# Optimization experiments

Measured on AMD Instinct MI355X. Metric: run time of the kernel, lower is better.

Reference implementation:

```python
import jax, jax.numpy as jnp
import numpy as np

DIM = 1024
N_HEADS = 16
HEAD_DIM = DIM // N_HEADS
D_FF = 4096
EPS = 1e-6


def setup_inputs() -> dict:
    key = jax.random.key(0)
    ks = jax.random.split(key, 8)
    B, S = 2, 2048
    s = 0.02
    return {
        "x": jax.random.normal(ks[0], (B, S, DIM), dtype=jnp.float32),
        "mask": jnp.ones((B, 1, S, S), dtype=bool),
        "wq": jax.random.normal(ks[1], (DIM, DIM), dtype=jnp.float32) * s,
        "wk": jax.random.normal(ks[2], (DIM, DIM), dtype=jnp.float32) * s,
        "wv": jax.random.normal(ks[3], (DIM, DIM), dtype=jnp.float32) * s,
        "wo": jax.random.normal(ks[4], (DIM, DIM), dtype=jnp.float32) * s,
        "w_up": jax.random.normal(ks[5], (DIM, D_FF), dtype=jnp.float32) * s,
        "b_up": jnp.zeros((D_FF,), dtype=jnp.float32),
        "w_down": jax.random.normal(ks[6], (D_FF, DIM), dtype=jnp.float32) * s,
        "b_down": jnp.zeros((DIM,), dtype=jnp.float32),
        "ln1_a": jnp.ones((DIM,), dtype=jnp.float32),
        "ln1_b": jnp.zeros((DIM,), dtype=jnp.float32),
        "ln2_a": jnp.ones((DIM,), dtype=jnp.float32),
        "ln2_b": jnp.zeros((DIM,), dtype=jnp.float32),
    }


def _layernorm(x, alpha, bias):
    mu = jnp.mean(x, axis=-1, keepdims=True)
    # torch .std() is unbiased (ddof=1); denominator is (std + eps)
    sig = jnp.std(x, axis=-1, keepdims=True, ddof=1)
    return alpha * (x - mu) / (sig + EPS) + bias


def _attention(h, wq, wk, wv, wo):
    B, S, _ = h.shape
    q = (h @ wq).reshape(B, S, N_HEADS, HEAD_DIM).transpose(0, 2, 1, 3)
    k = (h @ wk).reshape(B, S, N_HEADS, HEAD_DIM).transpose(0, 2, 1, 3)
    v = (h @ wv).reshape(B, S, N_HEADS, HEAD_DIM).transpose(0, 2, 1, 3)
    scores = jnp.einsum("bhqd,bhkd->bhqk", q, k) / jnp.sqrt(jnp.float32(HEAD_DIM))
    # NOTE: original's masked_fill result is discarded -> mask is a no-op
    probs = jax.nn.softmax(scores, axis=-1)
    out = jnp.einsum("bhqk,bhkd->bhqd", probs, v)
    out = out.transpose(0, 2, 1, 3).reshape(B, S, DIM)
    return out @ wo


def reference(x, mask, wq, wk, wv, wo, w_up, b_up, w_down, b_down,
              ln1_a, ln1_b, ln2_a, ln2_b):
    h = _layernorm(x, ln1_a, ln1_b)
    x = x + _attention(h, wq, wk, wv, wo)
    h = _layernorm(x, ln2_a, ln2_b)
    ff = (jax.nn.relu(h @ w_up + b_up)) @ w_down + b_down
    return x + ff
```

## Files before the change

### kernel.cpp

```cpp
#include <hip/hip_runtime.h>
#include <hip/hip_bf16.h>

typedef __bf16 bf16_t;
typedef __bf16 bf16x8 __attribute__((ext_vector_type(8)));
typedef __bf16 bf16x4 __attribute__((ext_vector_type(4)));
typedef float  f32x4  __attribute__((ext_vector_type(4)));

#define DIM   1024
#define NHEAD 16
#define HD    64
#define DFF   4096
#define SEQ   2048
#define NTOK  4096

__device__ __forceinline__ void gl_lds16(const bf16_t* g, bf16_t* l) {
  __builtin_amdgcn_global_load_lds(
      (const __attribute__((address_space(1))) void*)g,
      (__attribute__((address_space(3))) void*)l, 16, 0, 0);
}

struct P4 { const float* a; const float* b; const float* c; const float* d; };

__global__ __launch_bounds__(256)
void transpose_cvt4(P4 in, bf16_t* __restrict__ out) {
  __shared__ bf16_t tile[32][33];
  const int z = blockIdx.z;
  const float* src = (z == 0) ? in.a : (z == 1) ? in.b : (z == 2) ? in.c : in.d;
  bf16_t* dst = out + (long)z * DIM * DIM;
  const int bx = blockIdx.x * 32, by = blockIdx.y * 32;
  const int t = threadIdx.x;
  const int r = t >> 3, c4 = (t & 7) * 4;
  f32x4 v = *(const f32x4*)&src[(long)(by + r) * DIM + bx + c4];
  tile[r][c4 + 0] = (bf16_t)v[0]; tile[r][c4 + 1] = (bf16_t)v[1];
  tile[r][c4 + 2] = (bf16_t)v[2]; tile[r][c4 + 3] = (bf16_t)v[3];
  __syncthreads();
  bf16x4 w;
  w[0] = tile[c4 + 0][r]; w[1] = tile[c4 + 1][r];
  w[2] = tile[c4 + 2][r]; w[3] = tile[c4 + 3][r];
  *(bf16x4*)&dst[(long)(bx + r) * DIM + by + c4] = w;
}

__global__ __launch_bounds__(256)
void transpose_cvt(const float* __restrict__ in, bf16_t* __restrict__ out,
                   int M, int N) {
  __shared__ bf16_t tile[32][33];
  const int bx = blockIdx.x * 32, by = blockIdx.y * 32;
  const int t = threadIdx.x;
  const int r = t >> 3, c4 = (t & 7) * 4;
  f32x4 v = *(const f32x4*)&in[(long)(by + r) * N + bx + c4];
  tile[r][c4 + 0] = (bf16_t)v[0]; tile[r][c4 + 1] = (bf16_t)v[1];
  tile[r][c4 + 2] = (bf16_t)v[2]; tile[r][c4 + 3] = (bf16_t)v[3];
  __syncthreads();
  bf16x4 w;
  w[0] = tile[c4 + 0][r]; w[1] = tile[c4 + 1][r];
  w[2] = tile[c4 + 2][r]; w[3] = tile[c4 + 3][r];
  *(bf16x4*)&out[(long)(bx + r) * M + by + c4] = w;
}

__global__ __launch_bounds__(256)
void layernorm_k(const float* __restrict__ x, const float* __restrict__ a,
                 const float* __restrict__ b, bf16_t* __restrict__ out) {
  const int row = blockIdx.x;
  const int t   = threadIdx.x;
  const float* xr = x + (long)row * DIM;
  f32x4 v = *(const f32x4*)&xr[t * 4];
  float s1 = v[0] + v[1] + v[2] + v[3];
  float s2 = v[0]*v[0] + v[1]*v[1] + v[2]*v[2] + v[3]*v[3];
  #pragma unroll
  for (int off = 32; off > 0; off >>= 1) {
    s1 += __shfl_down(s1, off);
    s2 += __shfl_down(s2, off);
  }
  __shared__ float r1[4], r2[4];
  if ((t & 63) == 0) { r1[t >> 6] = s1; r2[t >> 6] = s2; }
  __syncthreads();
  s1 = r1[0] + r1[1] + r1[2] + r1[3];
  s2 = r2[0] + r2[1] + r2[2] + r2[3];
  const float mu = s1 * (1.0f / DIM);
  float var = (s2 - (float)DIM * mu * mu) * (1.0f / (DIM - 1));
  var = fmaxf(var, 0.0f);
  const float inv = 1.0f / (sqrtf(var) + 1e-6f);
  f32x4 av = *(const f32x4*)&a[t * 4];
  f32x4 bv = *(const f32x4*)&b[t * 4];
  bf16x4 o;
  o[0] = (bf16_t)(av[0] * (v[0] - mu) * inv + bv[0]);
  o[1] = (bf16_t)(av[1] * (v[1] - mu) * inv + bv[1]);
  o[2] = (bf16_t)(av[2] * (v[2] - mu) * inv + bv[2]);
  o[3] = (bf16_t)(av[3] * (v[3] - mu) * inv + bv[3]);
  *(bf16x4*)&out[(long)row * DIM + t * 4] = o;
}

enum { EPI_QKV = 1, EPI_RES = 2, EPI_BIAS_RELU = 3, EPI_BIAS_RES = 4 };

#define BM 128
#define BK 32

template <int EPI, int TBN>
__global__ __launch_bounds__(256)
void gemm_bt(const bf16_t* __restrict__ A, int lda,
             const bf16_t* __restrict__ BT, int ldb,
             bf16_t* __restrict__ Cb, float* __restrict__ Cf,
             bf16_t* __restrict__ Cb2,
             const float* __restrict__ res,
             const float* __restrict__ bias,
             int M, int N, int K) {
  __shared__ bf16_t sA[2][BM][BK];
  __shared__ bf16_t sB[2][TBN][BK];
  const int tid  = threadIdx.x;
  const int m0   = blockIdx.y * BM;
  const int n0   = blockIdx.x * TBN;
  const int lane = tid & 63, wave = tid >> 6;
  constexpr int MI = (TBN == 128) ? 4 : 2;
  const int wm = (TBN == 128) ? (wave >> 1) * 64 : wave * 32;
  const int wn = (TBN == 128) ? (wave & 1) * 64 : 0;
  const int fm = lane & 15, fq = lane >> 4;

  const int lr = lane >> 2, lc = (lane & 3) * 8;
  const bf16_t* gA0 = &A[(long)(m0 + wave * 32 + lr) * lda + lc];
  const bf16_t* gA1 = gA0 + 16 * (long)lda;
  const int brow = (TBN == 128) ? wave * 32 : wave * 16;
  const bf16_t* gB0 = &BT[(long)(n0 + brow + lr) * ldb + lc];
  const bf16_t* gB1 = gB0 + 16 * (long)ldb;

  f32x4 acc[MI][4] = {};

  gl_lds16(gA0, &sA[0][wave * 32][0]);
  gl_lds16(gA1, &sA[0][wave * 32 + 16][0]);
  gl_lds16(gB0, &sB[0][brow][0]);
  if (TBN == 128) gl_lds16(gB1, &sB[0][wave * 32 + 16][0]);
  gA0 += BK; gA1 += BK; gB0 += BK; gB1 += BK;

  int p = 0;
  for (int k0 = 0; k0 < K; k0 += BK, p ^= 1) {
    __syncthreads();
    if (k0 + BK < K) {
      gl_lds16(gA0, &sA[p ^ 1][wave * 32][0]);
      gl_lds16(gA1, &sA[p ^ 1][wave * 32 + 16][0]);
      gl_lds16(gB0, &sB[p ^ 1][brow][0]);
      if (TBN == 128) gl_lds16(gB1, &sB[p ^ 1][wave * 32 + 16][0]);
      gA0 += BK; gA1 += BK; gB0 += BK; gB1 += BK;
    }
    bf16x8 af[MI], bfr[4];
    #pragma unroll
    for (int i = 0; i < MI; i++) af[i]  = *(const bf16x8*)&sA[p][wm + i * 16 + fm][fq * 8];
    #pragma unroll
    for (int j = 0; j < 4; j++)  bfr[j] = *(const bf16x8*)&sB[p][wn + j * 16 + fm][fq * 8];
    #pragma unroll
    for (int i = 0; i < MI; i++)
      #pragma unroll
      for (int j = 0; j < 4; j++)
        acc[i][j] = __builtin_amdgcn_mfma_f32_16x16x32_bf16(af[i], bfr[j], acc[i][j], 0, 0, 0);
  }

  #pragma unroll
  for (int i = 0; i < MI; i++) {
    #pragma unroll
    for (int j = 0; j < 4; j++) {
      const int mb = m0 + wm + i * 16 + fq * 4;
      const int n  = n0 + wn + j * 16 + fm;
      #pragma unroll
      for (int r = 0; r < 4; r++) {
        const int m = mb + r;
        float vv = acc[i][j][r];
        if constexpr (EPI == EPI_QKV) {
          const int mat = n >> 10, h_ = (n >> 6) & 15, d_ = n & 63;
          const int b_ = m >> 11, s_ = m & 2047;
          if (mat == 2) {
            Cb2[((long)(b_ * NHEAD + h_) * HD + d_) * SEQ + s_] = (bf16_t)vv;
          } else {
            Cb[(long)mat * (32L * SEQ * HD) + (((long)(b_ * NHEAD + h_)) * SEQ + s_) * HD + d_] = (bf16_t)vv;
          }
        } else if constexpr (EPI == EPI_RES) {
          Cf[(long)m * N + n] = vv + res[(long)m * N + n];
        } else if constexpr (EPI == EPI_BIAS_RELU) {
          Cb[(long)m * N + n] = (bf16_t)fmaxf(vv + bias[n], 0.0f);
        } else {
          Cf[(long)m * N + n] = vv + bias[n] + res[(long)m * N + n];
        }
      }
    }
  }
}

#define KVT 128

__global__ __launch_bounds__(256)
void flash_attn(const bf16_t* __restrict__ q, const bf16_t* __restrict__ k,
                const bf16_t* __restrict__ vt, bf16_t* __restrict__ attn) {
  __shared__ bf16_t sK[16 * 64 * 8];
  __shared__ bf16_t sV[16 * 64 * 8];

  const int tid  = threadIdx.x;
  const int qb   = blockIdx.x & 15, bh = blockIdx.x >> 4;
  const int b    = bh >> 4, h = bh & 15;
  const int lane = tid & 63, wave = tid >> 6;
  const int fm   = lane & 15, fq = lane >> 4;
  const int qw0  = qb * 128 + wave * 32;

  const bf16_t* qh  = q  + (long)bh * SEQ * HD;
  const bf16_t* kh  = k  + (long)bh * SEQ * HD;
  const bf16_t* vth = vt + (long)bh * HD * SEQ;

  bf16x8 bQ[2][2];
  #pragma unroll
  for (int qt = 0; qt < 2; qt++)
    #pragma unroll
    for (int kk = 0; kk < 2; kk++) {
      bf16x8 v = *(const bf16x8*)&qh[(long)(qw0 + qt * 16 + fm) * HD + kk * 32 + fq * 8];
      #pragma unroll
      for (int e = 0; e < 8; e++) v[e] = (bf16_t)((float)v[e] * 0.125f);
      bQ[qt][kk] = v;
    }

  float la = 0.f, lb = 0.f;
  f32x4 oA[4] = {}, oB[4] = {};

  for (int kv0 = 0; kv0 < SEQ; kv0 += KVT) {
    __syncthreads();
    #pragma unroll
    for (int p = 0; p < 4; p++) {
      const int id = tid + p * 256;
      {
        const int rho = id >> 3, c0 = (id & 7) * 8;
        const int u = rho >> 5, w = rho & 31;
        const int h2 = (w >> 2) & 1;
        const int fmw = ((w >> 3) << 2) | (w & 3);
        const int kk = (id >> 2) & 1, fq3 = id & 3;
        bf16x8 g = *(const bf16x8*)&kh[(long)(kv0 + rho) * HD + c0];
        *(bf16x8*)&sK[(((u * 2 + h2) * 2 + kk) * 64 + fq3 * 16 + fmw) * 8] = g;
      }
      {
        const int d = id >> 4, c0 = (id & 15) * 8;
        const int u = c0 >> 5, fq3 = (c0 >> 3) & 3;
        const int jd = d >> 4, fmw = d & 15;
        bf16x8 g = *(const bf16x8*)&vth[(long)d * SEQ + kv0 + c0];
        *(bf16x8*)&sV[((u * 4 + jd) * 64 + fq3 * 16 + fmw) * 8] = g;
      }
    }
    __syncthreads();

    #pragma unroll
    for (int u = 0; u < 4; u++) {
      f32x4 stA[2], stB[2];
      #pragma unroll
      for (int h2 = 0; h2 < 2; h2++) {
        bf16x8 aK0 = *(const bf16x8*)&sK[(((u * 2 + h2) * 2 + 0) * 64 + lane) * 8];
        bf16x8 aK1 = *(const bf16x8*)&sK[(((u * 2 + h2) * 2 + 1) * 64 + lane) * 8];
        f32x4 z0 = {};
        z0 = __builtin_amdgcn_mfma_f32_16x16x32_bf16(aK0, bQ[0][0], z0, 0, 0, 0);
        stA[h2] = __builtin_amdgcn_mfma_f32_16x16x32_bf16(aK1, bQ[0][1], z0, 0, 0, 0);
        f32x4 z1 = {};
        z1 = __builtin_amdgcn_mfma_f32_16x16x32_bf16(aK0, bQ[1][0], z1, 0, 0, 0);
        stB[h2] = __builtin_amdgcn_mfma_f32_16x16x32_bf16(aK1, bQ[1][1], z1, 0, 0, 0);
      }
      bf16x8 pA, pB;
      #pragma unroll
      for (int h2 = 0; h2 < 2; h2++)
        #pragma unroll
        for (int r = 0; r < 4; r++) {
          const float ea = __expf(stA[h2][r]);
          const float eb = __expf(stB[h2][r]);
          la += ea; lb += eb;
          pA[h2 * 4 + r] = (bf16_t)ea;
          pB[h2 * 4 + r] = (bf16_t)eb;
        }
      #pragma unroll
      for (int jd = 0; jd < 4; jd++) {
        bf16x8 bV = *(const bf16x8*)&sV[((u * 4 + jd) * 64 + lane) * 8];
        oA[jd] = __builtin_amdgcn_mfma_f32_16x16x32_bf16(pA, bV, oA[jd], 0, 0, 0);
        oB[jd] = __builtin_amdgcn_mfma_f32_16x16x32_bf16(pB, bV, oB[jd], 0, 0, 0);
      }
    }
  }

  la += __shfl_xor(la, 16); la += __shfl_xor(la, 32);
  lb += __shfl_xor(lb, 16); lb += __shfl_xor(lb, 32);
  float invA[4], invB[4];
  #pragma unroll
  for (int r = 0; r < 4; r++) {
    const int src = (fq * 4 + r) * 4;
    invA[r] = 1.0f / __int_as_float(__builtin_amdgcn_ds_bpermute(src, __float_as_int(la)));
    invB[r] = 1.0f / __int_as_float(__builtin_amdgcn_ds_bpermute(src, __float_as_int(lb)));
  }

  #pragma unroll
  for (int r = 0; r < 4; r++) {
    const long rowA = ((long)b * SEQ + qw0 + fq * 4 + r) * DIM + h * HD;
    const long rowB = rowA + 16L * DIM;
    #pragma unroll
    for (int jd = 0; jd < 4; jd++) {
      attn[rowA + jd * 16 + fm] = (bf16_t)(oA[jd][r] * invA[r]);
      attn[rowB + jd * 16 + fm] = (bf16_t)(oB[jd][r] * invB[r]);
    }
  }
}

extern "C" void kernel_launch(void* const* d_in, const int* in_sizes, int n_in,
                              void* d_out, int out_size, void* d_ws, size_t ws_size,
                              hipStream_t stream) {
  (void)in_sizes; (void)n_in; (void)out_size; (void)ws_size;
  const float* x      = (const float*)d_in[0];
  const float* wq     = (const float*)d_in[2];
  const float* wk     = (const float*)d_in[3];
  const float* wv     = (const float*)d_in[4];
  const float* wo     = (const float*)d_in[5];
  const float* w_up   = (const float*)d_in[6];
  const float* b_up   = (const float*)d_in[7];
  const float* w_down = (const float*)d_in[8];
  const float* b_down = (const float*)d_in[9];
  const float* ln1a   = (const float*)d_in[10];
  const float* ln1b   = (const float*)d_in[11];
  const float* ln2a   = (const float*)d_in[12];
  const float* ln2b   = (const float*)d_in[13];

  char* ws = (char*)d_ws;
  const size_t MB = 1ull << 20;
  bf16_t* wqkvT  = (bf16_t*)(ws);
  bf16_t* woT    = (bf16_t*)(ws + 6 * MB);
  bf16_t* h      = (bf16_t*)(ws + 8 * MB);
  bf16_t* attn   = (bf16_t*)(ws + 8 * MB);
  bf16_t* qkv    = (bf16_t*)(ws + 16 * MB);
  bf16_t* qd     = (bf16_t*)(ws + 16 * MB);
  bf16_t* kd     = (bf16_t*)(ws + 24 * MB);
  bf16_t* vtd    = (bf16_t*)(ws + 32 * MB);
  float*  x1     = (float*)(ws + 40 * MB);
  bf16_t* h2     = (bf16_t*)(ws + 0 * MB);
  bf16_t* wupT   = (bf16_t*)(ws + 56 * MB);
  bf16_t* wdownT = (bf16_t*)(ws + 56 * MB);
  bf16_t* ff1    = (bf16_t*)(ws + 8 * MB);
  float*  outp   = (float*)d_out;

  const dim3 T(256);
  transpose_cvt4<<<dim3(32, 32, 4), T, 0, stream>>>(P4{wq, wk, wv, wo}, wqkvT);
  transpose_cvt<<<dim3(128, 32), T, 0, stream>>>(w_up, wupT, 1024, 4096);

  layernorm_k<<<dim3(4096), T, 0, stream>>>(x, ln1a, ln1b, h);
  gemm_bt<EPI_QKV, 128><<<dim3(24, 32), T, 0, stream>>>(h, DIM, wqkvT, DIM, qkv, nullptr,
                                                        vtd, nullptr, nullptr, NTOK, 3072, DIM);
  flash_attn<<<dim3(512), T, 0, stream>>>(qd, kd, vtd, attn);
  gemm_bt<EPI_RES, 64><<<dim3(16, 32), T, 0, stream>>>(attn, DIM, woT, DIM, nullptr, x1,
                                                       nullptr, x, nullptr, NTOK, DIM, DIM);
  layernorm_k<<<dim3(4096), T, 0, stream>>>(x1, ln2a, ln2b, h2);
  gemm_bt<EPI_BIAS_RELU, 128><<<dim3(32, 32), T, 0, stream>>>(h2, DIM, wupT, DIM, ff1, nullptr,
                                                              nullptr, nullptr, b_up, NTOK, DFF, DIM);
  transpose_cvt<<<dim3(32, 128), T, 0, stream>>>(w_down, wdownT, 4096, 1024);
  gemm_bt<EPI_BIAS_RES, 64><<<dim3(16, 32), T, 0, stream>>>(ff1, DFF, wdownT, DFF, nullptr, outp,
                                                            nullptr, x1, b_down, NTOK, DIM, DFF);
}
```

Before: 423.3 us.

## Split-K the N=1024 GEMMs with atomic accumulation into pre-initialised outputs

```diff
diff --git a/kernel.cpp b/kernel.cpp
--- a/kernel.cpp
+++ b/kernel.cpp
@@ -90,7 +90,17 @@
   *(bf16x4*)&out[(long)row * DIM + t * 4] = o;
 }
 
-enum { EPI_QKV = 1, EPI_RES = 2, EPI_BIAS_RELU = 3, EPI_BIAS_RES = 4 };
+__global__ __launch_bounds__(256)
+void init_bias(const float* __restrict__ x1, const float* __restrict__ bias,
+               float* __restrict__ out) {
+  const long i = ((long)blockIdx.x * 256 + threadIdx.x) * 4;
+  const int n = (int)(i & (DIM - 1));
+  f32x4 v = *(const f32x4*)&x1[i];
+  f32x4 bv = *(const f32x4*)&bias[n];
+  *(f32x4*)&out[i] = v + bv;
+}
+
+enum { EPI_QKV = 1, EPI_BIAS_RELU = 3, EPI_ATOM = 5 };
 
 #define BM 128
 #define BK 32
@@ -101,14 +111,14 @@
              const bf16_t* __restrict__ BT, int ldb,
              bf16_t* __restrict__ Cb, float* __restrict__ Cf,
              bf16_t* __restrict__ Cb2,
-             const float* __restrict__ res,
              const float* __restrict__ bias,
-             int M, int N, int K) {
+             int M, int N, int Ks) {
   __shared__ bf16_t sA[2][BM][BK];
   __shared__ bf16_t sB[2][TBN][BK];
   const int tid  = threadIdx.x;
   const int m0   = blockIdx.y * BM;
   const int n0   = blockIdx.x * TBN;
+  const long koff = (long)blockIdx.z * Ks;
   const int lane = tid & 63, wave = tid >> 6;
   constexpr int MI = (TBN == 128) ? 4 : 2;
   const int wm = (TBN == 128) ? (wave >> 1) * 64 : wave * 32;
@@ -116,10 +126,10 @@
   const int fm = lane & 15, fq = lane >> 4;
 
   const int lr = lane >> 2, lc = (lane & 3) * 8;
-  const bf16_t* gA0 = &A[(long)(m0 + wave * 32 + lr) * lda + lc];
+  const bf16_t* gA0 = &A[(long)(m0 + wave * 32 + lr) * lda + koff + lc];
   const bf16_t* gA1 = gA0 + 16 * (long)lda;
   const int brow = (TBN == 128) ? wave * 32 : wave * 16;
-  const bf16_t* gB0 = &BT[(long)(n0 + brow + lr) * ldb + lc];
+  const bf16_t* gB0 = &BT[(long)(n0 + brow + lr) * ldb + koff + lc];
   const bf16_t* gB1 = gB0 + 16 * (long)ldb;
 
   f32x4 acc[MI][4] = {};
@@ -131,9 +141,9 @@
   gA0 += BK; gA1 += BK; gB0 += BK; gB1 += BK;
 
   int p = 0;
-  for (int k0 = 0; k0 < K; k0 += BK, p ^= 1) {
+  for (int k0 = 0; k0 < Ks; k0 += BK, p ^= 1) {
     __syncthreads();
-    if (k0 + BK < K) {
+    if (k0 + BK < Ks) {
       gl_lds16(gA0, &sA[p ^ 1][wave * 32][0]);
       gl_lds16(gA1, &sA[p ^ 1][wave * 32 + 16][0]);
       gl_lds16(gB0, &sB[p ^ 1][brow][0]);
@@ -170,12 +180,10 @@
           } else {
             Cb[(long)mat * (32L * SEQ * HD) + (((long)(b_ * NHEAD + h_)) * SEQ + s_) * HD + d_] = (bf16_t)vv;
           }
-        } else if constexpr (EPI == EPI_RES) {
-          Cf[(long)m * N + n] = vv + res[(long)m * N + n];
         } else if constexpr (EPI == EPI_BIAS_RELU) {
           Cb[(long)m * N + n] = (bf16_t)fmaxf(vv + bias[n], 0.0f);
         } else {
-          Cf[(long)m * N + n] = vv + bias[n] + res[(long)m * N + n];
+          atomicAdd(&Cf[(long)m * N + n], vv);
         }
       }
     }
@@ -336,14 +344,17 @@
 
   layernorm_k<<<dim3(4096), T, 0, stream>>>(x, ln1a, ln1b, h);
   gemm_bt<EPI_QKV, 128><<<dim3(24, 32), T, 0, stream>>>(h, DIM, wqkvT, DIM, qkv, nullptr,
-                                                        vtd, nullptr, nullptr, NTOK, 3072, DIM);
+                                                        vtd, nullptr, NTOK, 3072, DIM);
   flash_attn<<<dim3(512), T, 0, stream>>>(qd, kd, vtd, attn);
-  gemm_bt<EPI_RES, 64><<<dim3(16, 32), T, 0, stream>>>(attn, DIM, woT, DIM, nullptr, x1,
-                                                       nullptr, x, nullptr, NTOK, DIM, DIM);
+  hipMemcpyAsync(x1, x, (size_t)NTOK * DIM * sizeof(float),
+                 hipMemcpyDeviceToDevice, stream);
+  gemm_bt<EPI_ATOM, 64><<<dim3(16, 32, 2), T, 0, stream>>>(attn, DIM, woT, DIM, nullptr, x1,
+                                                           nullptr, nullptr, NTOK, DIM, DIM / 2);
   layernorm_k<<<dim3(4096), T, 0, stream>>>(x1, ln2a, ln2b, h2);
   gemm_bt<EPI_BIAS_RELU, 128><<<dim3(32, 32), T, 0, stream>>>(h2, DIM, wupT, DIM, ff1, nullptr,
-                                                              nullptr, nullptr, b_up, NTOK, DFF, DIM);
+                                                              nullptr, b_up, NTOK, DFF, DIM);
   transpose_cvt<<<dim3(32, 128), T, 0, stream>>>(w_down, wdownT, 4096, 1024);
-  gemm_bt<EPI_BIAS_RES, 64><<<dim3(16, 32), T, 0, stream>>>(ff1, DFF, wdownT, DFF, nullptr, outp,
-                                                            nullptr, x1, b_down, NTOK, DIM, DFF);
-}
+  init_bias<<<dim3(NTOK * DIM / 1024), T, 0, stream>>>(x1, b_down, outp);
+  gemm_bt<EPI_ATOM, 64><<<dim3(16, 32, 4), T, 0, stream>>>(ff1, DFF, wdownT, DFF, nullptr, outp,
+                                                           nullptr, nullptr, NTOK, DIM, DFF / 4);
+}
```

After: 462.8 us. 1.09x slower.
